# Optimization experiments

Measured on AMD Instinct MI355X. Metric: run time of the kernel, lower is better.

## Reference

```python
import jax, jax.numpy as jnp
import numpy as np

D_MODEL = 1024
HEAD = 16
HEAD_DIM = D_MODEL // HEAD
BATCH = 2
SEQ = 2048


def setup_inputs() -> dict:
    key = jax.random.key(0)
    ks = jax.random.split(key, 11)
    s = 0.02
    return {
        "q": jax.random.normal(ks[0], (BATCH, SEQ, D_MODEL), dtype=jnp.float32),
        "k": jax.random.normal(ks[1], (BATCH, SEQ, D_MODEL), dtype=jnp.float32),
        "v": jax.random.normal(ks[2], (BATCH, SEQ, D_MODEL), dtype=jnp.float32),
        "w_q": jax.random.normal(ks[3], (D_MODEL, D_MODEL), dtype=jnp.float32) * s,
        "b_q": jnp.zeros((D_MODEL,), dtype=jnp.float32),
        "w_k": jax.random.normal(ks[4], (D_MODEL, D_MODEL), dtype=jnp.float32) * s,
        "b_k": jnp.zeros((D_MODEL,), dtype=jnp.float32),
        "w_v": jax.random.normal(ks[5], (D_MODEL, D_MODEL), dtype=jnp.float32) * s,
        "b_v": jnp.zeros((D_MODEL,), dtype=jnp.float32),
        "w_o": jax.random.normal(ks[6], (D_MODEL, D_MODEL), dtype=jnp.float32) * s,
        "b_o": jnp.zeros((D_MODEL,), dtype=jnp.float32),
    }


def reference(q, k, v, w_q, b_q, w_k, b_k, w_v, b_v, w_o, b_o):
    B, S, _ = q.shape
    # linear projections (torch Linear: x @ W^T + b)
    qp = q @ w_q.T + b_q
    kp = k @ w_k.T + b_k
    vp = v @ w_v.T + b_v
    # [B, S, H, Dh] -> [B, H, S, Dh]
    qh = qp.reshape(B, S, HEAD, HEAD_DIM).transpose(0, 2, 1, 3)
    kh = kp.reshape(B, S, HEAD, HEAD_DIM).transpose(0, 2, 1, 3)
    vh = vp.reshape(B, S, HEAD, HEAD_DIM).transpose(0, 2, 1, 3)
    # scaled dot-product attention with explicit score matrix
    scale = 1.0 / jnp.sqrt(jnp.float32(HEAD_DIM))
    scores = jnp.einsum("bhqd,bhkd->bhqk", qh, kh) * scale  # [B,H,S,S]
    attn = jax.nn.softmax(scores, axis=-1)
    z = jnp.einsum("bhqk,bhkd->bhqd", attn, vh)
    z = z.transpose(0, 2, 1, 3).reshape(B, S, D_MODEL)
    z = z @ w_o.T + b_o
    return (z, attn)
```

## Files before the change

### kernel.cpp

```cpp
#include <hip/hip_runtime.h>
#include <hip/hip_bf16.h>
#include <stdint.h>

#define D_MODEL 1024
#define NHEAD   16
#define HDIM    64
#define BATCH   2
#define SEQ     2048
#define BS_TOK  (BATCH*SEQ)

using bf16 = __hip_bfloat16;
typedef __attribute__((ext_vector_type(8))) short frag8;
typedef __attribute__((ext_vector_type(4))) float facc4;

__device__ __forceinline__ void gld_lds16(const void* g, void* l) {
    __builtin_amdgcn_global_load_lds(
        reinterpret_cast<const __attribute__((address_space(1))) uint32_t*>(
            reinterpret_cast<uintptr_t>(g)),
        reinterpret_cast<__attribute__((address_space(3))) uint32_t*>(
            reinterpret_cast<uintptr_t>(l)),
        16, 0, 0);
}

__device__ __forceinline__ void ldsbar() {
    asm volatile("s_waitcnt lgkmcnt(0)" ::: "memory");
    __builtin_amdgcn_sched_barrier(0);
    __builtin_amdgcn_s_barrier();
}

__global__ __launch_bounds__(256) void cvt_all(const float* __restrict__ q, const float* __restrict__ k,
                                               const float* __restrict__ v, const float* __restrict__ wq,
                                               const float* __restrict__ wk, const float* __restrict__ wv,
                                               const float* __restrict__ wo,
                                               ushort* __restrict__ dq, ushort* __restrict__ dk,
                                               ushort* __restrict__ dv, ushort* __restrict__ dwq,
                                               ushort* __restrict__ dwk, ushort* __restrict__ dwv,
                                               ushort* __restrict__ dwo,
                                               int nbt, int n4t, int nbw, int n4w) {
    int blk = blockIdx.x;
    const float4* s; ushort4* d; int i, n4;
    if (blk < 3 * nbt) {
        int t = blk / nbt;
        i = (blk - t * nbt) * 256 + threadIdx.x; n4 = n4t;
        s = (const float4*)(t == 0 ? q : t == 1 ? k : v);
        d = (ushort4*)(t == 0 ? dq : t == 1 ? dk : dv);
    } else {
        blk -= 3 * nbt;
        int t = blk / nbw;
        i = (blk - t * nbw) * 256 + threadIdx.x; n4 = n4w;
        s = (const float4*)(t == 0 ? wq : t == 1 ? wk : t == 2 ? wv : wo);
        d = (ushort4*)(t == 0 ? dwq : t == 1 ? dwk : t == 2 ? dwv : dwo);
    }
    if (i >= n4) return;
    float4 vv = s[i];
    bf16 a = __float2bfloat16(vv.x), b = __float2bfloat16(vv.y),
         c = __float2bfloat16(vv.z), e = __float2bfloat16(vv.w);
    ushort4 u;
    __builtin_memcpy(&u.x, &a, 2);
    __builtin_memcpy(&u.y, &b, 2);
    __builtin_memcpy(&u.z, &c, 2);
    __builtin_memcpy(&u.w, &e, 2);
    d[i] = u;
}

template<bool OUT_BF16, bool ROW_BIAS>
__device__ __forceinline__ void gemm_core(bf16* AsBuf, bf16* BsBuf,
                                          const bf16* __restrict__ A,
                                          const bf16* __restrict__ Bt,
                                          const float* __restrict__ bias,
                                          void* __restrict__ Cout,
                                          int M, int N, int K, int bx, int by) {
    const int tid  = threadIdx.x;
    const int lane = tid & 63, wave = tid >> 6;
    const int wm = wave >> 1, wn = wave & 1;
    const int L15 = lane & 15, quad = lane >> 4;
    const int m0 = by * 128, n0 = bx * 64;
    const int ar  = tid >> 3;
    const int acS = ((tid & 7) ^ (ar & 7)) * 8;

    const bf16* Agl[4];
    const bf16* Bgl[2];
#pragma unroll
    for (int q = 0; q < 4; q++) Agl[q] = A + (size_t)(m0 + q * 32 + ar) * K + acS;
#pragma unroll
    for (int q = 0; q < 2; q++) Bgl[q] = Bt + (size_t)(n0 + q * 32 + ar) * K + acS;

    const facc4 zero4 = {0.f, 0.f, 0.f, 0.f};
    facc4 acc[4][2];
#pragma unroll
    for (int mt = 0; mt < 4; mt++) { acc[mt][0] = zero4; acc[mt][1] = zero4; }

#define G_STAGE(BUF, KO) do {                                                   \
        _Pragma("unroll")                                                       \
        for (int q = 0; q < 4; q++)                                             \
            gld_lds16(Agl[q] + (KO), AsBuf + (BUF) * 8192 + q * 2048 + wave * 512); \
        _Pragma("unroll")                                                       \
        for (int q = 0; q < 2; q++)                                             \
            gld_lds16(Bgl[q] + (KO), BsBuf + (BUF) * 4096 + q * 2048 + wave * 512); \
    } while (0)

#define G_COMPUTE(BUF) do {                                                     \
        const bf16* Ab = AsBuf + (BUF) * 8192;                                  \
        const bf16* Bb = BsBuf + (BUF) * 4096;                                  \
        _Pragma("unroll")                                                       \
        for (int h = 0; h < 2; h++) {                                           \
            frag8 af[4], bfr[2];                                                \
            _Pragma("unroll")                                                   \
            for (int mt = 0; mt < 4; mt++) {                                    \
                int row = wm * 64 + mt * 16 + L15;                              \
                int c8 = (h * 4 + quad) ^ (row & 7);                            \
                af[mt] = *(const frag8*)(Ab + row * 64 + c8 * 8);               \
            }                                                                   \
            _Pragma("unroll")                                                   \
            for (int nt = 0; nt < 2; nt++) {                                    \
                int row = wn * 32 + nt * 16 + L15;                              \
                int c8 = (h * 4 + quad) ^ (row & 7);                            \
                bfr[nt] = *(const frag8*)(Bb + row * 64 + c8 * 8);              \
            }                                                                   \
            _Pragma("unroll")                                                   \
            for (int mt = 0; mt < 4; mt++)                                      \
                _Pragma("unroll")                                               \
                for (int nt = 0; nt < 2; nt++)                                  \
                    acc[mt][nt] = __builtin_amdgcn_mfma_f32_16x16x32_bf16(af[mt], bfr[nt], acc[mt][nt], 0, 0, 0); \
        }                                                                       \
    } while (0)

    G_STAGE(0, 0);
    __syncthreads();
    int cur = 0;
    for (int k0 = 64; k0 < K; k0 += 64) {
        G_STAGE(cur ^ 1, k0);
        G_COMPUTE(cur);
        __syncthreads();
        cur ^= 1;
    }
    G_COMPUTE(cur);

#pragma unroll
    for (int mt = 0; mt < 4; mt++)
#pragma unroll
        for (int nt = 0; nt < 2; nt++)
#pragma unroll
            for (int r = 0; r < 4; r++) {
                int row = m0 + wm * 64 + mt * 16 + quad * 4 + r;
                int col = n0 + wn * 32 + nt * 16 + L15;
                float v = acc[mt][nt][r] + (ROW_BIAS ? bias[row] : bias[col]);
                if (OUT_BF16) ((bf16*)Cout)[(size_t)row * N + col] = __float2bfloat16(v);
                else          ((float*)Cout)[(size_t)row * N + col] = v;
            }
#undef G_STAGE
#undef G_COMPUTE
}

__global__ __launch_bounds__(256) void proj_all(const bf16* __restrict__ qA, const bf16* __restrict__ Wq,
                                                const float* __restrict__ bq, bf16* __restrict__ qO,
                                                const bf16* __restrict__ kA, const bf16* __restrict__ Wk,
                                                const float* __restrict__ bk, bf16* __restrict__ kO,
                                                const bf16* __restrict__ Wv, const bf16* __restrict__ vA,
                                                const float* __restrict__ bv, bf16* __restrict__ vO) {
    __shared__ bf16 As[2 * 8192];
    __shared__ bf16 Bs[2 * 4096];
    int id = blockIdx.x;
    if (id < 512) {
        gemm_core<true, false>(As, Bs, qA, Wq, bq, qO, BS_TOK, D_MODEL, D_MODEL, id & 15, id >> 4);
    } else if (id < 1024) {
        id -= 512;
        gemm_core<true, false>(As, Bs, kA, Wk, bk, kO, BS_TOK, D_MODEL, D_MODEL, id & 15, id >> 4);
    } else {
        id -= 1024;
        gemm_core<true, true>(As, Bs, Wv, vA, bv, vO, D_MODEL, BS_TOK, D_MODEL, id & 63, id >> 6);
    }
}

template<bool OUT_BF16, bool ROW_BIAS>
__global__ __launch_bounds__(256) void gemm_bt(const bf16* __restrict__ A,
                                               const bf16* __restrict__ Bt,
                                               const float* __restrict__ bias,
                                               void* __restrict__ Cout,
                                               int M, int N, int K) {
    __shared__ bf16 As[2 * 8192];
    __shared__ bf16 Bs[2 * 4096];
    gemm_core<OUT_BF16, ROW_BIAS>(As, Bs, A, Bt, bias, Cout, M, N, K, blockIdx.x, blockIdx.y);
}

__device__ __forceinline__ int pidx2(int row, int col) {
    int chunk = col >> 3;
    return row * 512 + (((chunk ^ (row & 7)) << 3) | (col & 7));
}

__global__ __launch_bounds__(256) void attn_kernel(const bf16* __restrict__ qp,
                                                   const bf16* __restrict__ kp,
                                                   const bf16* __restrict__ vT,
                                                   bf16* __restrict__ zbuf,
                                                   float* __restrict__ attn_out) {
    __shared__ bf16 ptile[2][16 * 512];
    __shared__ float sred[4][16];
    __shared__ float sinv[16];
    const int bid0 = blockIdx.x;
    const int bid = (bid0 & 7) * 512 + (bid0 >> 3);
    const int strip = bid & 127, bh = bid >> 7;
    const int b = bh >> 4, h = bh & 15;
    const int i0 = strip * 16;
    const int tid = threadIdx.x, lane = tid & 63, wave = tid >> 6;
    const int L15 = lane & 15, quad = lane >> 4;
    const float scale = 0.125f;

    frag8 aq0, aq1;
    {
        size_t base = (size_t)(b * SEQ + i0 + L15) * D_MODEL + h * HDIM + quad * 8;
        aq0 = *(const frag8*)(qp + base);
        aq1 = *(const frag8*)(qp + base + 32);
    }
    const facc4 zero4 = {0.f, 0.f, 0.f, 0.f};

    float sums[4] = {0.f, 0.f, 0.f, 0.f};
    for (int tt = 0; tt < 32; tt += 2) {
        int j0a = wave * 512 + tt * 16;
        size_t kba = (size_t)(b * SEQ + j0a + L15) * D_MODEL + h * HDIM + quad * 8;
        frag8 a0 = *(const frag8*)(kp + kba);
        frag8 a1 = *(const frag8*)(kp + kba + 32);
        frag8 c0 = *(const frag8*)(kp + kba + (size_t)16 * D_MODEL);
        frag8 c1 = *(const frag8*)(kp + kba + (size_t)16 * D_MODEL + 32);
        facc4 acca = zero4, accb = zero4;
        acca = __builtin_amdgcn_mfma_f32_16x16x32_bf16(aq0, a0, acca, 0, 0, 0);
        accb = __builtin_amdgcn_mfma_f32_16x16x32_bf16(aq0, c0, accb, 0, 0, 0);
        acca = __builtin_amdgcn_mfma_f32_16x16x32_bf16(aq1, a1, acca, 0, 0, 0);
        accb = __builtin_amdgcn_mfma_f32_16x16x32_bf16(aq1, c1, accb, 0, 0, 0);
#pragma unroll
        for (int r = 0; r < 4; r++)
            sums[r] += __expf(acca[r] * scale) + __expf(accb[r] * scale);
    }
#pragma unroll
    for (int m = 1; m <= 8; m <<= 1)
#pragma unroll
        for (int r = 0; r < 4; r++) sums[r] += __shfl_xor(sums[r], m, 64);
    if (L15 == 0) {
#pragma unroll
        for (int r = 0; r < 4; r++) sred[wave][quad * 4 + r] = sums[r];
    }
    __syncthreads();
    if (tid < 16) sinv[tid] = 1.0f / (sred[0][tid] + sred[1][tid] + sred[2][tid] + sred[3][tid]);
    __syncthreads();

    float invr[4];
#pragma unroll
    for (int r = 0; r < 4; r++) invr[r] = sinv[quad * 4 + r];

    facc4 zacc = zero4;
    const bf16* vrow = vT + (size_t)(h * HDIM + wave * 16 + L15) * BS_TOK + b * SEQ;
    const size_t obase = ((size_t)bh * SEQ + i0) * SEQ;

#define ATT_STAGE(CHK, BUF) do {                                                     \
        _Pragma("unroll")                                                            \
        for (int tt = 0; tt < 8; tt++) {                                             \
            int jrel = wave * 128 + tt * 16;                                         \
            int j0 = (CHK) * 512 + jrel;                                             \
            size_t kb = (size_t)(b * SEQ + j0 + L15) * D_MODEL + h * HDIM + quad * 8;\
            frag8 kf0 = *(const frag8*)(kp + kb);                                    \
            frag8 kf1 = *(const frag8*)(kp + kb + 32);                               \
            facc4 acc = zero4;                                                       \
            acc = __builtin_amdgcn_mfma_f32_16x16x32_bf16(aq0, kf0, acc, 0, 0, 0);   \
            acc = __builtin_amdgcn_mfma_f32_16x16x32_bf16(aq1, kf1, acc, 0, 0, 0);   \
            int colw = jrel + L15;                                                   \
            _Pragma("unroll")                                                        \
            for (int r = 0; r < 4; r++) {                                            \
                int row = quad * 4 + r;                                              \
                float a = __expf(acc[r] * scale) * invr[r];                          \
                attn_out[obase + (size_t)row * SEQ + j0 + L15] = a;                  \
                ptile[BUF][pidx2(row, colw)] = __float2bfloat16(a);                  \
            }                                                                        \
        }                                                                            \
    } while (0)

#define ATT_PV(CHK, BUF) do {                                                        \
        _Pragma("unroll")                                                            \
        for (int k0 = 0; k0 < 512; k0 += 32) {                                       \
            frag8 pa = *(const frag8*)&ptile[BUF][L15 * 512 +                        \
                        ((((k0 >> 3) + quad) ^ (L15 & 7)) << 3)];                    \
            frag8 vb = *(const frag8*)(vrow + (CHK) * 512 + k0 + quad * 8);          \
            zacc = __builtin_amdgcn_mfma_f32_16x16x32_bf16(pa, vb, zacc, 0, 0, 0);   \
        }                                                                            \
    } while (0)

    ATT_STAGE(0, 0);
    ldsbar();
    ATT_STAGE(1, 1); ATT_PV(0, 0);
    ldsbar();
    ATT_STAGE(2, 0); ATT_PV(1, 1);
    ldsbar();
    ATT_STAGE(3, 1); ATT_PV(2, 0);
    ldsbar();
    ATT_PV(3, 1);
#undef ATT_STAGE
#undef ATT_PV

#pragma unroll
    for (int r = 0; r < 4; r++) {
        size_t row = (size_t)(b * SEQ + i0 + quad * 4 + r);
        zbuf[row * D_MODEL + h * HDIM + wave * 16 + L15] = __float2bfloat16(zacc[r]);
    }
}

extern "C" void kernel_launch(void* const* d_in, const int* in_sizes, int n_in,
                              void* d_out, int out_size, void* d_ws, size_t ws_size,
                              hipStream_t stream) {
    const float* q   = (const float*)d_in[0];
    const float* k   = (const float*)d_in[1];
    const float* v   = (const float*)d_in[2];
    const float* w_q = (const float*)d_in[3];
    const float* b_q = (const float*)d_in[4];
    const float* w_k = (const float*)d_in[5];
    const float* b_k = (const float*)d_in[6];
    const float* w_v = (const float*)d_in[7];
    const float* b_v = (const float*)d_in[8];
    const float* w_o = (const float*)d_in[9];
    const float* b_o = (const float*)d_in[10];

    char* ws = (char*)d_ws;
    const size_t TOK = (size_t)BS_TOK * D_MODEL;
    const size_t WM  = (size_t)D_MODEL * D_MODEL;
    bf16* qbf  = (bf16*)(ws);
    bf16* kbf  = (bf16*)(ws + 8388608);
    bf16* vbf  = (bf16*)(ws + 16777216);
    bf16* wqb  = (bf16*)(ws + 25165824);
    bf16* wkb  = (bf16*)(ws + 27262976);
    bf16* wvb  = (bf16*)(ws + 29360128);
    bf16* wob  = (bf16*)(ws + 31457280);
    bf16* qp   = (bf16*)(ws + 33554432);
    bf16* kp   = (bf16*)(ws + 41943040);
    bf16* vT   = (bf16*)(ws + 50331648);
    bf16* zbf  = (bf16*)(ws + 58720256);

    float* z_out    = (float*)d_out;
    float* attn_out = (float*)d_out + (size_t)BATCH * SEQ * D_MODEL;

    int n4t = (int)(TOK / 4), n4w = (int)(WM / 4);
    int nbt = (n4t + 255) / 256, nbw = (n4w + 255) / 256;
    cvt_all<<<3 * nbt + 4 * nbw, 256, 0, stream>>>(q, k, v, w_q, w_k, w_v, w_o,
                                                   (ushort*)qbf, (ushort*)kbf, (ushort*)vbf,
                                                   (ushort*)wqb, (ushort*)wkb, (ushort*)wvb,
                                                   (ushort*)wob, nbt, n4t, nbw, n4w);

    proj_all<<<1536, 256, 0, stream>>>(qbf, wqb, b_q, qp,
                                       kbf, wkb, b_k, kp,
                                       wvb, vbf, b_v, vT);

    attn_kernel<<<BATCH * NHEAD * (SEQ / 16), 256, 0, stream>>>(qp, kp, vT, zbf, attn_out);

    dim3 g1(D_MODEL / 64, BS_TOK / 128);
    gemm_bt<false, false><<<g1, 256, 0, stream>>>(zbf, wob, b_o, z_out, BS_TOK, D_MODEL, D_MODEL);
}
```

Before: 960.7 us.

## Process 32 query rows per attention block to reuse K and V loads

Each attention block now handles two 16-row query strips, so every K fragment and V fragment loaded from global memory feeds two MFMAs instead of one. This halves redundant K/V traffic and halves the grid size. The double-buffered LDS pipeline is replaced by a single P tile with two __syncthreads per chunk, and launch bounds now request 4 blocks per CU. The cost is more registers and lost overlap between the score stage and the PV stage. The kernel is likely dominated by the 512MB fp32 attention write, so the gain may be limited.

```diff
diff --git a/kernel.cpp b/kernel.cpp
--- a/kernel.cpp
+++ b/kernel.cpp
@@ -20,12 +20,6 @@
         reinterpret_cast<__attribute__((address_space(3))) uint32_t*>(
             reinterpret_cast<uintptr_t>(l)),
         16, 0, 0);
-}
-
-__device__ __forceinline__ void ldsbar() {
-    asm volatile("s_waitcnt lgkmcnt(0)" ::: "memory");
-    __builtin_amdgcn_sched_barrier(0);
-    __builtin_amdgcn_s_barrier();
 }
 
 __global__ __launch_bounds__(256) void cvt_all(const float* __restrict__ q, const float* __restrict__ k,
@@ -188,117 +182,119 @@
     return row * 512 + (((chunk ^ (row & 7)) << 3) | (col & 7));
 }
 
-__global__ __launch_bounds__(256) void attn_kernel(const bf16* __restrict__ qp,
-                                                   const bf16* __restrict__ kp,
-                                                   const bf16* __restrict__ vT,
-                                                   bf16* __restrict__ zbuf,
-                                                   float* __restrict__ attn_out) {
-    __shared__ bf16 ptile[2][16 * 512];
-    __shared__ float sred[4][16];
-    __shared__ float sinv[16];
+__global__ __launch_bounds__(256, 4) void attn_kernel(const bf16* __restrict__ qp,
+                                                      const bf16* __restrict__ kp,
+                                                      const bf16* __restrict__ vT,
+                                                      bf16* __restrict__ zbuf,
+                                                      float* __restrict__ attn_out) {
+    __shared__ bf16 ptile[32 * 512];
+    __shared__ float sred[4][32];
+    __shared__ float sinv[32];
     const int bid0 = blockIdx.x;
-    const int bid = (bid0 & 7) * 512 + (bid0 >> 3);
-    const int strip = bid & 127, bh = bid >> 7;
+    const int bid = (bid0 & 7) * 256 + (bid0 >> 3);
+    const int strip = bid & 63, bh = bid >> 6;
     const int b = bh >> 4, h = bh & 15;
-    const int i0 = strip * 16;
+    const int i0 = strip * 32;
     const int tid = threadIdx.x, lane = tid & 63, wave = tid >> 6;
     const int L15 = lane & 15, quad = lane >> 4;
     const float scale = 0.125f;
 
-    frag8 aq0, aq1;
-    {
-        size_t base = (size_t)(b * SEQ + i0 + L15) * D_MODEL + h * HDIM + quad * 8;
-        aq0 = *(const frag8*)(qp + base);
-        aq1 = *(const frag8*)(qp + base + 32);
+    frag8 aq[2][2];
+#pragma unroll
+    for (int s = 0; s < 2; s++) {
+        size_t base = (size_t)(b * SEQ + i0 + s * 16 + L15) * D_MODEL + h * HDIM + quad * 8;
+        aq[s][0] = *(const frag8*)(qp + base);
+        aq[s][1] = *(const frag8*)(qp + base + 32);
     }
     const facc4 zero4 = {0.f, 0.f, 0.f, 0.f};
 
-    float sums[4] = {0.f, 0.f, 0.f, 0.f};
-    for (int tt = 0; tt < 32; tt += 2) {
-        int j0a = wave * 512 + tt * 16;
-        size_t kba = (size_t)(b * SEQ + j0a + L15) * D_MODEL + h * HDIM + quad * 8;
-        frag8 a0 = *(const frag8*)(kp + kba);
-        frag8 a1 = *(const frag8*)(kp + kba + 32);
-        frag8 c0 = *(const frag8*)(kp + kba + (size_t)16 * D_MODEL);
-        frag8 c1 = *(const frag8*)(kp + kba + (size_t)16 * D_MODEL + 32);
-        facc4 acca = zero4, accb = zero4;
-        acca = __builtin_amdgcn_mfma_f32_16x16x32_bf16(aq0, a0, acca, 0, 0, 0);
-        accb = __builtin_amdgcn_mfma_f32_16x16x32_bf16(aq0, c0, accb, 0, 0, 0);
-        acca = __builtin_amdgcn_mfma_f32_16x16x32_bf16(aq1, a1, acca, 0, 0, 0);
-        accb = __builtin_amdgcn_mfma_f32_16x16x32_bf16(aq1, c1, accb, 0, 0, 0);
-#pragma unroll
-        for (int r = 0; r < 4; r++)
-            sums[r] += __expf(acca[r] * scale) + __expf(accb[r] * scale);
+    float sums[2][4] = {{0.f, 0.f, 0.f, 0.f}, {0.f, 0.f, 0.f, 0.f}};
+    for (int tt = 0; tt < 32; tt++) {
+        int j0 = wave * 512 + tt * 16;
+        size_t kb = (size_t)(b * SEQ + j0 + L15) * D_MODEL + h * HDIM + quad * 8;
+        frag8 kf0 = *(const frag8*)(kp + kb);
+        frag8 kf1 = *(const frag8*)(kp + kb + 32);
+        facc4 a0 = zero4, a1 = zero4;
+        a0 = __builtin_amdgcn_mfma_f32_16x16x32_bf16(aq[0][0], kf0, a0, 0, 0, 0);
+        a1 = __builtin_amdgcn_mfma_f32_16x16x32_bf16(aq[1][0], kf0, a1, 0, 0, 0);
+        a0 = __builtin_amdgcn_mfma_f32_16x16x32_bf16(aq[0][1], kf1, a0, 0, 0, 0);
+        a1 = __builtin_amdgcn_mfma_f32_16x16x32_bf16(aq[1][1], kf1, a1, 0, 0, 0);
+#pragma unroll
+        for (int r = 0; r < 4; r++) {
+            sums[0][r] += __expf(a0[r] * scale);
+            sums[1][r] += __expf(a1[r] * scale);
+        }
     }
 #pragma unroll
     for (int m = 1; m <= 8; m <<= 1)
 #pragma unroll
-        for (int r = 0; r < 4; r++) sums[r] += __shfl_xor(sums[r], m, 64);
+        for (int s = 0; s < 2; s++)
+#pragma unroll
+            for (int r = 0; r < 4; r++) sums[s][r] += __shfl_xor(sums[s][r], m, 64);
     if (L15 == 0) {
 #pragma unroll
-        for (int r = 0; r < 4; r++) sred[wave][quad * 4 + r] = sums[r];
+        for (int s = 0; s < 2; s++)
+#pragma unroll
+            for (int r = 0; r < 4; r++) sred[wave][s * 16 + quad * 4 + r] = sums[s][r];
     }
     __syncthreads();
-    if (tid < 16) sinv[tid] = 1.0f / (sred[0][tid] + sred[1][tid] + sred[2][tid] + sred[3][tid]);
+    if (tid < 32) sinv[tid] = 1.0f / (sred[0][tid] + sred[1][tid] + sred[2][tid] + sred[3][tid]);
     __syncthreads();
 
-    float invr[4];
-#pragma unroll
-    for (int r = 0; r < 4; r++) invr[r] = sinv[quad * 4 + r];
-
-    facc4 zacc = zero4;
+    float invr[2][4];
+#pragma unroll
+    for (int s = 0; s < 2; s++)
+#pragma unroll
+        for (int r = 0; r < 4; r++) invr[s][r] = sinv[s * 16 + quad * 4 + r];
+
+    facc4 zacc[2] = {zero4, zero4};
     const bf16* vrow = vT + (size_t)(h * HDIM + wave * 16 + L15) * BS_TOK + b * SEQ;
     const size_t obase = ((size_t)bh * SEQ + i0) * SEQ;
 
-#define ATT_STAGE(CHK, BUF) do {                                                     \
-        _Pragma("unroll")                                                            \
-        for (int tt = 0; tt < 8; tt++) {                                             \
-            int jrel = wave * 128 + tt * 16;                                         \
-            int j0 = (CHK) * 512 + jrel;                                             \
-            size_t kb = (size_t)(b * SEQ + j0 + L15) * D_MODEL + h * HDIM + quad * 8;\
-            frag8 kf0 = *(const frag8*)(kp + kb);                                    \
-            frag8 kf1 = *(const frag8*)(kp + kb + 32);                               \
-            facc4 acc = zero4;                                                       \
-            acc = __builtin_amdgcn_mfma_f32_16x16x32_bf16(aq0, kf0, acc, 0, 0, 0);   \
-            acc = __builtin_amdgcn_mfma_f32_16x16x32_bf16(aq1, kf1, acc, 0, 0, 0);   \
-            int colw = jrel + L15;                                                   \
-            _Pragma("unroll")                                                        \
-            for (int r = 0; r < 4; r++) {                                            \
-                int row = quad * 4 + r;                                              \
-                float a = __expf(acc[r] * scale) * invr[r];                          \
-                attn_out[obase + (size_t)row * SEQ + j0 + L15] = a;                  \
-                ptile[BUF][pidx2(row, colw)] = __float2bfloat16(a);                  \
-            }                                                                        \
-        }                                                                            \
-    } while (0)
-
-#define ATT_PV(CHK, BUF) do {                                                        \
-        _Pragma("unroll")                                                            \
-        for (int k0 = 0; k0 < 512; k0 += 32) {                                       \
-            frag8 pa = *(const frag8*)&ptile[BUF][L15 * 512 +                        \
-                        ((((k0 >> 3) + quad) ^ (L15 & 7)) << 3)];                    \
-            frag8 vb = *(const frag8*)(vrow + (CHK) * 512 + k0 + quad * 8);          \
-            zacc = __builtin_amdgcn_mfma_f32_16x16x32_bf16(pa, vb, zacc, 0, 0, 0);   \
-        }                                                                            \
-    } while (0)
-
-    ATT_STAGE(0, 0);
-    ldsbar();
-    ATT_STAGE(1, 1); ATT_PV(0, 0);
-    ldsbar();
-    ATT_STAGE(2, 0); ATT_PV(1, 1);
-    ldsbar();
-    ATT_STAGE(3, 1); ATT_PV(2, 0);
-    ldsbar();
-    ATT_PV(3, 1);
-#undef ATT_STAGE
-#undef ATT_PV
-
-#pragma unroll
-    for (int r = 0; r < 4; r++) {
-        size_t row = (size_t)(b * SEQ + i0 + quad * 4 + r);
-        zbuf[row * D_MODEL + h * HDIM + wave * 16 + L15] = __float2bfloat16(zacc[r]);
-    }
+    for (int c = 0; c < 4; c++) {
+#pragma unroll 2
+        for (int tt = 0; tt < 8; tt++) {
+            int jrel = wave * 128 + tt * 16;
+            int j0 = c * 512 + jrel;
+            size_t kb = (size_t)(b * SEQ + j0 + L15) * D_MODEL + h * HDIM + quad * 8;
+            frag8 kf0 = *(const frag8*)(kp + kb);
+            frag8 kf1 = *(const frag8*)(kp + kb + 32);
+            facc4 a0 = zero4, a1 = zero4;
+            a0 = __builtin_amdgcn_mfma_f32_16x16x32_bf16(aq[0][0], kf0, a0, 0, 0, 0);
+            a1 = __builtin_amdgcn_mfma_f32_16x16x32_bf16(aq[1][0], kf0, a1, 0, 0, 0);
+            a0 = __builtin_amdgcn_mfma_f32_16x16x32_bf16(aq[0][1], kf1, a0, 0, 0, 0);
+            a1 = __builtin_amdgcn_mfma_f32_16x16x32_bf16(aq[1][1], kf1, a1, 0, 0, 0);
+            int colw = jrel + L15;
+#pragma unroll
+            for (int r = 0; r < 4; r++) {
+                int row0 = quad * 4 + r;
+                float p0 = __expf(a0[r] * scale) * invr[0][r];
+                float p1 = __expf(a1[r] * scale) * invr[1][r];
+                attn_out[obase + (size_t)row0 * SEQ + j0 + L15] = p0;
+                attn_out[obase + (size_t)(row0 + 16) * SEQ + j0 + L15] = p1;
+                ptile[pidx2(row0, colw)] = __float2bfloat16(p0);
+                ptile[pidx2(row0 + 16, colw)] = __float2bfloat16(p1);
+            }
+        }
+        __syncthreads();
+#pragma unroll 4
+        for (int k0 = 0; k0 < 512; k0 += 32) {
+            int sw = ((((k0 >> 3) + quad) ^ (L15 & 7)) << 3);
+            frag8 pa0 = *(const frag8*)&ptile[L15 * 512 + sw];
+            frag8 pa1 = *(const frag8*)&ptile[(L15 + 16) * 512 + sw];
+            frag8 vb = *(const frag8*)(vrow + c * 512 + k0 + quad * 8);
+            zacc[0] = __builtin_amdgcn_mfma_f32_16x16x32_bf16(pa0, vb, zacc[0], 0, 0, 0);
+            zacc[1] = __builtin_amdgcn_mfma_f32_16x16x32_bf16(pa1, vb, zacc[1], 0, 0, 0);
+        }
+        __syncthreads();
+    }
+#pragma unroll
+    for (int s = 0; s < 2; s++)
+#pragma unroll
+        for (int r = 0; r < 4; r++) {
+            size_t row = (size_t)(b * SEQ + i0 + s * 16 + quad * 4 + r);
+            zbuf[row * D_MODEL + h * HDIM + wave * 16 + L15] = __float2bfloat16(zacc[s][r]);
+        }
 }
 
 extern "C" void kernel_launch(void* const* d_in, const int* in_sizes, int n_in,
@@ -345,7 +341,7 @@
                                        kbf, wkb, b_k, kp,
                                        wvb, vbf, b_v, vT);
 
-    attn_kernel<<<BATCH * NHEAD * (SEQ / 16), 256, 0, stream>>>(qp, kp, vT, zbf, attn_out);
+    attn_kernel<<<BATCH * NHEAD * (SEQ / 32), 256, 0, stream>>>(qp, kp, vT, zbf, attn_out);
 
     dim3 g1(D_MODEL / 64, BS_TOK / 128);
     gemm_bt<false, false><<<g1, 256, 0, stream>>>(zbf, wob, b_o, z_out, BS_TOK, D_MODEL, D_MODEL);
```

Result: faster. 816.4 us (-15.0%).
